# Performance work log

Hardware: AMD Instinct MI355X
Metric: run time of the kernel (lower is better)

The kernel has to match this reference:

```python
import jax, jax.numpy as jnp
import numpy as np

N_NODES = 100000


def setup_inputs() -> dict:
    key = jax.random.key(0)
    k1, k2, k3 = jax.random.split(key, 3)
    x = jax.random.normal(k1, (N_NODES, 128), dtype=jnp.float32)
    edge_index = jax.random.randint(k2, (2, 1600000), 0, N_NODES, dtype=jnp.int64)
    # GCNConv linear weight (hidden, input) and bias; PReLU slope (init 0.25 as in torch)
    W = jax.random.normal(k3, (128, 128), dtype=jnp.float32) * (1.0 / np.sqrt(128))
    b = jnp.zeros((128,), dtype=jnp.float32)
    prelu_a = jnp.full((1,), 0.25, dtype=jnp.float32)
    return {"x": x, "edge_index": edge_index, "W": W, "b": b, "prelu_a": prelu_a}


def reference(x, edge_index, W, b, prelu_a):
    n = x.shape[0]
    # add self loops (as in forward's add_self_loops)
    loop = jnp.arange(n, dtype=edge_index.dtype)
    src = jnp.concatenate([edge_index[0], loop])  # [E+N]
    dst = jnp.concatenate([edge_index[1], loop])
    # linear transform first (small GEMM), then gather/scatter on hidden dim
    h = x @ W.T  # [N, H]
    # symmetric degree normalization 1/sqrt(deg_src * deg_dst), deg = in-degree incl. self-loop
    ones = jnp.ones_like(dst, dtype=h.dtype)
    deg = jax.ops.segment_sum(ones, dst, num_segments=n)
    dinv = jnp.where(deg > 0, jax.lax.rsqrt(deg), 0.0)  # [N]
    norm = dinv[src] * dinv[dst]  # [E+N]
    msg = h[src] * norm[:, None]  # gather + scale, memory-bound
    out = jax.ops.segment_sum(msg, dst, num_segments=n) + b  # scatter-add
    # PReLU (single shared slope); dropout is identity in eval mode
    out = jnp.where(out >= 0, out, prelu_a[0] * out)
    return out
```

## Files before the change

### kernel.cpp

```cpp
#include <hip/hip_runtime.h>
#include <math.h>

#define HDIM 128
#define BSH 9
#define CH 4096
#define GEMM_BLKS 256
#define GSPLIT 160

typedef __attribute__((ext_vector_type(8))) short short8;
typedef __attribute__((ext_vector_type(4))) float f32x4;

__device__ inline unsigned short bf16_hi(float f) {
    return (unsigned short)(__float_as_uint(f) >> 16);
}
__device__ inline unsigned short bf16_rn(float f) {
    unsigned int u = __float_as_uint(f);
    return (unsigned short)((u + 0x7FFF + ((u >> 16) & 1)) >> 16);
}

__global__ __launch_bounds__(256) void prep_kernel(
    const float* __restrict__ W, uint4* __restrict__ Whg, uint4* __restrict__ Wlg) {
    const int t = threadIdx.x;
    for (int idx = t; idx < 2048; idx += 256) {
        const int j = idx >> 4;
        const int c = idx & 15;
        const float4* wp = (const float4*)(W + (size_t)j * HDIM + c * 8);
        float4 va = wp[0], vb = wp[1];
        float vs[8] = {va.x, va.y, va.z, va.w, vb.x, vb.y, vb.z, vb.w};
        unsigned short h[8], l[8];
        #pragma unroll
        for (int k = 0; k < 8; ++k) {
            h[k] = bf16_hi(vs[k]);
            float hf = __uint_as_float((unsigned int)h[k] << 16);
            l[k] = bf16_hi(vs[k] - hf);
        }
        uint4 hch, lch;
        hch.x = (unsigned int)h[0] | ((unsigned int)h[1] << 16);
        hch.y = (unsigned int)h[2] | ((unsigned int)h[3] << 16);
        hch.z = (unsigned int)h[4] | ((unsigned int)h[5] << 16);
        hch.w = (unsigned int)h[6] | ((unsigned int)h[7] << 16);
        lch.x = (unsigned int)l[0] | ((unsigned int)l[1] << 16);
        lch.y = (unsigned int)l[2] | ((unsigned int)l[3] << 16);
        lch.z = (unsigned int)l[4] | ((unsigned int)l[5] << 16);
        lch.w = (unsigned int)l[6] | ((unsigned int)l[7] << 16);
        Whg[idx] = hch;
        Wlg[idx] = lch;
    }
}

__device__ __forceinline__ void gemm_body(
    const float* __restrict__ x, const uint4* __restrict__ Whg,
    const uint4* __restrict__ Wlg, unsigned short* __restrict__ gb, int n,
    int g0, int g1, int bid, int nblk) {
    const int t = threadIdx.x;
    const int wave = t >> 6;
    const int lane = t & 63;
    const int q = lane >> 4;
    const int m = lane & 15;

    for (int grp = g0 + bid; grp < g1; grp += nblk) {
        const int rowbase = (grp << 7) + (wave << 5);

        f32x4 acc[2][8];
        #pragma unroll
        for (int mt = 0; mt < 2; ++mt)
            #pragma unroll
            for (int ct = 0; ct < 8; ++ct)
                acc[mt][ct] = (f32x4){0.f, 0.f, 0.f, 0.f};

        #pragma unroll
        for (int kk = 0; kk < 4; ++kk) {
            short8 ah[2], al[2];
            #pragma unroll
            for (int mt = 0; mt < 2; ++mt) {
                const int r = rowbase + (mt << 4) + m;
                float vs[8];
                if (r < n) {
                    const float4* xp = (const float4*)(x + (size_t)r * HDIM + (kk << 5) + (q << 3));
                    float4 va = xp[0], vb = xp[1];
                    vs[0] = va.x; vs[1] = va.y; vs[2] = va.z; vs[3] = va.w;
                    vs[4] = vb.x; vs[5] = vb.y; vs[6] = vb.z; vs[7] = vb.w;
                } else {
                    #pragma unroll
                    for (int k = 0; k < 8; ++k) vs[k] = 0.f;
                }
                #pragma unroll
                for (int k = 0; k < 8; ++k) {
                    unsigned short h = bf16_hi(vs[k]);
                    float hf = __uint_as_float((unsigned int)h << 16);
                    unsigned short lo = bf16_hi(vs[k] - hf);
                    ah[mt][k] = (short)h;
                    al[mt][k] = (short)lo;
                }
            }
            #pragma unroll
            for (int ct = 0; ct < 8; ++ct) {
                const int nn = (ct << 4) + m;
                const int fidx = (nn << 4) | ((kk << 2) + q);
                short8 bh = *(const short8*)&Whg[fidx];
                short8 bl = *(const short8*)&Wlg[fidx];
                #pragma unroll
                for (int mt = 0; mt < 2; ++mt) {
                    acc[mt][ct] = __builtin_amdgcn_mfma_f32_16x16x32_bf16(ah[mt], bh, acc[mt][ct], 0, 0, 0);
                    acc[mt][ct] = __builtin_amdgcn_mfma_f32_16x16x32_bf16(al[mt], bh, acc[mt][ct], 0, 0, 0);
                    acc[mt][ct] = __builtin_amdgcn_mfma_f32_16x16x32_bf16(ah[mt], bl, acc[mt][ct], 0, 0, 0);
                }
            }
        }

        #pragma unroll
        for (int mt = 0; mt < 2; ++mt) {
            #pragma unroll
            for (int rr = 0; rr < 4; ++rr) {
                const int grow = rowbase + (mt << 4) + (q << 2) + rr;
                if (grow < n) {
                    unsigned short* gp = gb + (size_t)grow * HDIM + m;
                    #pragma unroll
                    for (int ct = 0; ct < 8; ++ct)
                        gp[ct << 4] = bf16_rn(acc[mt][ct][rr]);
                }
            }
        }
    }
}

__device__ __forceinline__ void binA_body(
    const int* __restrict__ dst, int E, int* __restrict__ bcnt,
    int chunk, int* hist) {
    const int t = threadIdx.x;
    const int c0 = chunk * CH;
    hist[t] = 0;
    __syncthreads();
    #pragma unroll
    for (int k = 0; k < CH / 256; ++k) {
        int e = c0 + t + (k << 8);
        if (e < E) atomicAdd(&hist[dst[e] >> BSH], 1);
    }
    __syncthreads();
    if (hist[t] > 0) atomicAdd(&bcnt[t], hist[t]);
}

__device__ __forceinline__ void binB_body(
    const int* __restrict__ ei, int E,
    int* __restrict__ bcur, unsigned int* __restrict__ eb,
    int chunk, int* hist, int* base, int* cur) {
    const int t = threadIdx.x;
    const int c0 = chunk * CH;
    hist[t] = 0;
    __syncthreads();

    int sv[CH / 256], dv[CH / 256];
    #pragma unroll
    for (int k = 0; k < CH / 256; ++k) {
        int e = c0 + t + (k << 8);
        if (e < E) {
            sv[k] = ei[e];
            dv[k] = ei[E + e];
            atomicAdd(&hist[dv[k] >> BSH], 1);
        } else {
            dv[k] = -1;
        }
    }
    __syncthreads();
    if (hist[t] > 0) base[t] = atomicAdd(&bcur[t], hist[t]);
    cur[t] = 0;
    __syncthreads();
    #pragma unroll
    for (int k = 0; k < CH / 256; ++k) {
        if (dv[k] >= 0) {
            int bkt = dv[k] >> BSH;
            int o = atomicAdd(&cur[bkt], 1);
            eb[(size_t)base[bkt] + o] =
                ((unsigned int)(dv[k] & ((1 << BSH) - 1)) << 23) | (unsigned int)sv[k];
        }
    }
}

__global__ __launch_bounds__(256) void fuse1_kernel(
    const int* __restrict__ dst, int E, int* __restrict__ bcnt,
    const float* __restrict__ x, const uint4* __restrict__ Whg,
    const uint4* __restrict__ Wlg, unsigned short* __restrict__ gb,
    int n, int nchunk) {
    __shared__ int s_a[256];
    const int bid = blockIdx.x;
    if (bid < GEMM_BLKS)
        gemm_body(x, Whg, Wlg, gb, n, 0, GSPLIT, bid, GEMM_BLKS);
    else
        binA_body(dst, E, bcnt, bid - GEMM_BLKS, s_a);
}

__global__ __launch_bounds__(256) void scanB_kernel(
    const int* __restrict__ bcnt, int* __restrict__ bbase, int* __restrict__ bcur,
    int NB, int E) {
    __shared__ int s[256];
    const int t = threadIdx.x;
    int v = (t < NB) ? bcnt[t] : 0;
    s[t] = v;
    __syncthreads();
    for (int off = 1; off < 256; off <<= 1) {
        int u = (t >= off) ? s[t - off] : 0;
        __syncthreads();
        s[t] += u;
        __syncthreads();
    }
    int excl = s[t] - v;
    if (t < NB) { bbase[t] = excl; bcur[t] = excl; }
    if (t == 0) bbase[NB] = E;
}

__global__ __launch_bounds__(256) void fuse2_kernel(
    const int* __restrict__ ei, int E, int* __restrict__ bcur,
    unsigned int* __restrict__ eb,
    const float* __restrict__ x, const uint4* __restrict__ Whg,
    const uint4* __restrict__ Wlg, unsigned short* __restrict__ gb,
    int n, int nchunk, int ngroups) {
    __shared__ int s_a[256], s_b[256], s_c[256];
    const int bid = blockIdx.x;
    if (bid < GEMM_BLKS)
        gemm_body(x, Whg, Wlg, gb, n, GSPLIT, ngroups, bid, GEMM_BLKS);
    else
        binB_body(ei, E, bcur, eb, bid - GEMM_BLKS, s_a, s_b, s_c);
}

__global__ __launch_bounds__(512) void binC_kernel(
    const unsigned int* __restrict__ eb, const int* __restrict__ bbase,
    int* __restrict__ row_ptr, float* __restrict__ dinv,
    int* __restrict__ col, int n) {
    __shared__ int hist[512];
    __shared__ int cur[512];
    __shared__ int wsum[8];
    const int t = threadIdx.x;
    const int b = blockIdx.x;
    const int node0 = b << BSH;
    const int e0 = bbase[b];
    const int e1 = bbase[b + 1];

    hist[t] = 0;
    __syncthreads();
    for (int e = e0 + t; e < e1; e += 512)
        atomicAdd(&hist[eb[e] >> 23], 1);
    __syncthreads();
    const int v = hist[t];
    int x = v;
    #pragma unroll
    for (int off = 1; off < 64; off <<= 1) {
        int u = __shfl_up(x, off);
        if ((t & 63) >= off) x += u;
    }
    if ((t & 63) == 63) wsum[t >> 6] = x;
    __syncthreads();
    if (t < 8) {
        int y = wsum[t];
        #pragma unroll
        for (int off = 1; off < 8; off <<= 1) {
            int u = __shfl_up(y, off);
            if (t >= off) y += u;
        }
        wsum[t] = y;
    }
    __syncthreads();
    int excl = x - v + ((t >> 6) ? wsum[(t >> 6) - 1] : 0);

    int node = node0 + t;
    if (node < n) {
        row_ptr[node] = e0 + excl;
        dinv[node] = rsqrtf((float)v + 1.0f);
        if (node == n - 1) row_ptr[n] = e0 + excl + v;
    }
    cur[t] = e0 + excl;
    __syncthreads();
    for (int e = e0 + t; e < e1; e += 512) {
        unsigned int p = eb[e];
        int pos = atomicAdd(&cur[p >> 23], 1);
        col[pos] = (int)(p & 0x7FFFFF);
    }
}

#define EDGE_ACC(d, u) \
    a[0] = fmaf(d, __uint_as_float((u).x << 16), a[0]); \
    a[1] = fmaf(d, __uint_as_float((u).x & 0xffff0000u), a[1]); \
    a[2] = fmaf(d, __uint_as_float((u).y << 16), a[2]); \
    a[3] = fmaf(d, __uint_as_float((u).y & 0xffff0000u), a[3]); \
    a[4] = fmaf(d, __uint_as_float((u).z << 16), a[4]); \
    a[5] = fmaf(d, __uint_as_float((u).z & 0xffff0000u), a[5]); \
    a[6] = fmaf(d, __uint_as_float((u).w << 16), a[6]); \
    a[7] = fmaf(d, __uint_as_float((u).w & 0xffff0000u), a[7]);

__global__ __launch_bounds__(256) void gather_kernel(
    const int* __restrict__ row_ptr, const int* __restrict__ col,
    const uint4* __restrict__ gbr, const float* __restrict__ dinv,
    const float* __restrict__ bias, const float* __restrict__ prelu_a,
    float* __restrict__ out, int n) {
    const int wv = threadIdx.x >> 6;
    const int lane = threadIdx.x & 63;
    const int q = lane >> 4;
    const int l16 = lane & 15;
    const int i = blockIdx.x * 4 + wv;
    if (i >= n) return;

    const int beg = row_ptr[i];
    const int end = row_ptr[i + 1];
    const float di = dinv[i];

    float a[8];
    #pragma unroll
    for (int k = 0; k < 8; ++k) a[k] = 0.f;

    if (q == 0) {
        uint4 u = gbr[(size_t)i * 16 + l16];
        EDGE_ACC(di, u)
    }

    int e = beg + q;
    for (; e + 12 < end; e += 16) {
        int s0 = col[e];
        int s1 = col[e + 4];
        int s2 = col[e + 8];
        int s3 = col[e + 12];
        float d0 = dinv[s0], d1 = dinv[s1], d2 = dinv[s2], d3 = dinv[s3];
        uint4 u0 = gbr[(size_t)s0 * 16 + l16];
        uint4 u1 = gbr[(size_t)s1 * 16 + l16];
        uint4 u2 = gbr[(size_t)s2 * 16 + l16];
        uint4 u3 = gbr[(size_t)s3 * 16 + l16];
        EDGE_ACC(d0, u0)
        EDGE_ACC(d1, u1)
        EDGE_ACC(d2, u2)
        EDGE_ACC(d3, u3)
    }
    for (; e + 4 < end; e += 8) {
        int s0 = col[e];
        int s1 = col[e + 4];
        float d0 = dinv[s0], d1 = dinv[s1];
        uint4 u0 = gbr[(size_t)s0 * 16 + l16];
        uint4 u1 = gbr[(size_t)s1 * 16 + l16];
        EDGE_ACC(d0, u0)
        EDGE_ACC(d1, u1)
    }
    if (e < end) {
        int s = col[e];
        float d = dinv[s];
        uint4 u = gbr[(size_t)s * 16 + l16];
        EDGE_ACC(d, u)
    }

    #pragma unroll
    for (int k = 0; k < 8; ++k) {
        a[k] += __shfl_xor(a[k], 16);
        a[k] += __shfl_xor(a[k], 32);
    }

    const float aa = prelu_a[0];
    const int c0 = (l16 << 3) + (q << 1);
    float2 bb = *(const float2*)(bias + c0);
    float v0 = di * a[(q << 1) + 0] + bb.x;
    float v1 = di * a[(q << 1) + 1] + bb.y;
    v0 = v0 >= 0.f ? v0 : aa * v0;
    v1 = v1 >= 0.f ? v1 : aa * v1;
    *(float2*)(out + (size_t)i * HDIM + c0) = make_float2(v0, v1);
}

extern "C" void kernel_launch(void* const* d_in, const int* in_sizes, int n_in,
                              void* d_out, int out_size, void* d_ws, size_t ws_size,
                              hipStream_t stream) {
    const float* x  = (const float*)d_in[0];
    const int*   ei = (const int*)d_in[1];
    const float* W  = (const float*)d_in[2];
    const float* b  = (const float*)d_in[3];
    const float* pa = (const float*)d_in[4];

    const int n = in_sizes[0] / HDIM;
    const int E = in_sizes[1] / 2;
    const int NB = (n + (1 << BSH) - 1) >> BSH;
    const int ngroups = (n + 127) >> 7;

    float* out = (float*)d_out;

    unsigned short* gb      = (unsigned short*)d_ws;
    unsigned int*   eb      = (unsigned int*)(gb + (size_t)n * HDIM);
    uint4*          Whg     = (uint4*)(eb + (size_t)E);
    uint4*          Wlg     = Whg + 2048;
    float*          dinv    = (float*)(Wlg + 2048);
    int*            row_ptr = (int*)(dinv + n);
    int*            col     = row_ptr + (n + 1);
    int*            bcnt    = col + E;
    int*            bbase   = bcnt + 256;
    int*            bcur    = bbase + 257;

    hipMemsetAsync(bcnt, 0, 256 * sizeof(int), stream);

    const int nchunk = (E + CH - 1) / CH;
    prep_kernel<<<1, 256, 0, stream>>>(W, Whg, Wlg);
    fuse1_kernel<<<GEMM_BLKS + nchunk, 256, 0, stream>>>(ei + E, E, bcnt, x, Whg, Wlg, gb, n, nchunk);
    scanB_kernel<<<1, 256, 0, stream>>>(bcnt, bbase, bcur, NB, E);
    fuse2_kernel<<<GEMM_BLKS + nchunk, 256, 0, stream>>>(ei, E, bcur, eb, x, Whg, Wlg, gb, n, nchunk, ngroups);
    binC_kernel<<<NB, 512, 0, stream>>>(eb, bbase, row_ptr, dinv, col, n);
    gather_kernel<<<(n + 3) / 4, 256, 0, stream>>>(row_ptr, col, (const uint4*)gb, dinv, b, pa, out, n);
}
```

Before: 252.9 us.

## Remove scan kernel by recomputing bucket prefix in binning blocks; halve bucket size

```diff
diff --git a/kernel.cpp b/kernel.cpp
--- a/kernel.cpp
+++ b/kernel.cpp
@@ -2,7 +2,8 @@
 #include <math.h>
 
 #define HDIM 128
-#define BSH 9
+#define BSH 8
+#define LSH 24
 #define CH 4096
 #define GEMM_BLKS 256
 #define GSPLIT 160
@@ -130,6 +131,7 @@
     const int t = threadIdx.x;
     const int c0 = chunk * CH;
     hist[t] = 0;
+    hist[t + 256] = 0;
     __syncthreads();
     #pragma unroll
     for (int k = 0; k < CH / 256; ++k) {
@@ -138,15 +140,17 @@
     }
     __syncthreads();
     if (hist[t] > 0) atomicAdd(&bcnt[t], hist[t]);
+    if (hist[t + 256] > 0) atomicAdd(&bcnt[t + 256], hist[t + 256]);
 }
 
 __device__ __forceinline__ void binB_body(
-    const int* __restrict__ ei, int E,
-    int* __restrict__ bcur, unsigned int* __restrict__ eb,
-    int chunk, int* hist, int* base, int* cur) {
+    const int* __restrict__ ei, int E, const int* __restrict__ bcnt,
+    int* __restrict__ boff, unsigned int* __restrict__ eb,
+    int chunk, int* hist, int* bb, int* base, int* cur, int NB) {
     const int t = threadIdx.x;
     const int c0 = chunk * CH;
     hist[t] = 0;
+    hist[t + 256] = 0;
     __syncthreads();
 
     int sv[CH / 256], dv[CH / 256];
@@ -162,16 +166,38 @@
         }
     }
     __syncthreads();
-    if (hist[t] > 0) base[t] = atomicAdd(&bcur[t], hist[t]);
+
+    if (t < 64) {
+        int carry = 0;
+        #pragma unroll
+        for (int c = 0; c < 512; c += 64) {
+            int idx = c + t;
+            int v = (idx < NB) ? bcnt[idx] : 0;
+            int xs = v;
+            #pragma unroll
+            for (int off = 1; off < 64; off <<= 1) {
+                int u = __shfl_up(xs, off);
+                if (t >= off) xs += u;
+            }
+            bb[idx] = carry + xs - v;
+            carry += __shfl(xs, 63);
+        }
+    }
+    __syncthreads();
+
+    if (hist[t] > 0)       base[t]       = bb[t]       + atomicAdd(&boff[t],       hist[t]);
+    if (hist[t + 256] > 0) base[t + 256] = bb[t + 256] + atomicAdd(&boff[t + 256], hist[t + 256]);
     cur[t] = 0;
-    __syncthreads();
+    cur[t + 256] = 0;
+    __syncthreads();
+
     #pragma unroll
     for (int k = 0; k < CH / 256; ++k) {
         if (dv[k] >= 0) {
             int bkt = dv[k] >> BSH;
             int o = atomicAdd(&cur[bkt], 1);
             eb[(size_t)base[bkt] + o] =
-                ((unsigned int)(dv[k] & ((1 << BSH) - 1)) << 23) | (unsigned int)sv[k];
+                ((unsigned int)(dv[k] & ((1 << BSH) - 1)) << LSH) | (unsigned int)sv[k];
         }
     }
 }
@@ -179,9 +205,8 @@
 __global__ __launch_bounds__(256) void fuse1_kernel(
     const int* __restrict__ dst, int E, int* __restrict__ bcnt,
     const float* __restrict__ x, const uint4* __restrict__ Whg,
-    const uint4* __restrict__ Wlg, unsigned short* __restrict__ gb,
-    int n, int nchunk) {
-    __shared__ int s_a[256];
+    const uint4* __restrict__ Wlg, unsigned short* __restrict__ gb, int n) {
+    __shared__ int s_a[512];
     const int bid = blockIdx.x;
     if (bid < GEMM_BLKS)
         gemm_body(x, Whg, Wlg, gb, n, 0, GSPLIT, bid, GEMM_BLKS);
@@ -189,56 +214,48 @@
         binA_body(dst, E, bcnt, bid - GEMM_BLKS, s_a);
 }
 
-__global__ __launch_bounds__(256) void scanB_kernel(
-    const int* __restrict__ bcnt, int* __restrict__ bbase, int* __restrict__ bcur,
-    int NB, int E) {
-    __shared__ int s[256];
-    const int t = threadIdx.x;
-    int v = (t < NB) ? bcnt[t] : 0;
-    s[t] = v;
-    __syncthreads();
-    for (int off = 1; off < 256; off <<= 1) {
-        int u = (t >= off) ? s[t - off] : 0;
-        __syncthreads();
-        s[t] += u;
-        __syncthreads();
-    }
-    int excl = s[t] - v;
-    if (t < NB) { bbase[t] = excl; bcur[t] = excl; }
-    if (t == 0) bbase[NB] = E;
-}
-
 __global__ __launch_bounds__(256) void fuse2_kernel(
-    const int* __restrict__ ei, int E, int* __restrict__ bcur,
-    unsigned int* __restrict__ eb,
+    const int* __restrict__ ei, int E, const int* __restrict__ bcnt,
+    int* __restrict__ boff, unsigned int* __restrict__ eb,
     const float* __restrict__ x, const uint4* __restrict__ Whg,
     const uint4* __restrict__ Wlg, unsigned short* __restrict__ gb,
-    int n, int nchunk, int ngroups) {
-    __shared__ int s_a[256], s_b[256], s_c[256];
+    int n, int ngroups, int NB) {
+    __shared__ int s_h[512], s_bb[512], s_ba[512], s_cu[512];
     const int bid = blockIdx.x;
     if (bid < GEMM_BLKS)
         gemm_body(x, Whg, Wlg, gb, n, GSPLIT, ngroups, bid, GEMM_BLKS);
     else
-        binB_body(ei, E, bcur, eb, bid - GEMM_BLKS, s_a, s_b, s_c);
-}
-
-__global__ __launch_bounds__(512) void binC_kernel(
-    const unsigned int* __restrict__ eb, const int* __restrict__ bbase,
+        binB_body(ei, E, bcnt, boff, eb, bid - GEMM_BLKS, s_h, s_bb, s_ba, s_cu, NB);
+}
+
+__global__ __launch_bounds__(256) void binC_kernel(
+    const unsigned int* __restrict__ eb, const int* __restrict__ bcnt,
     int* __restrict__ row_ptr, float* __restrict__ dinv,
-    int* __restrict__ col, int n) {
-    __shared__ int hist[512];
-    __shared__ int cur[512];
-    __shared__ int wsum[8];
+    int* __restrict__ col, int n, int NB) {
+    __shared__ int hist[256];
+    __shared__ int cur[256];
+    __shared__ int red[256];
+    __shared__ int wsum[4];
     const int t = threadIdx.x;
     const int b = blockIdx.x;
     const int node0 = b << BSH;
-    const int e0 = bbase[b];
-    const int e1 = bbase[b + 1];
+
+    int part = 0;
+    for (int k = t; k < b; k += 256) part += bcnt[k];
+    red[t] = part;
+    __syncthreads();
+    #pragma unroll
+    for (int off = 128; off > 0; off >>= 1) {
+        if (t < off) red[t] += red[t + off];
+        __syncthreads();
+    }
+    const int e0 = red[0];
+    const int e1 = e0 + bcnt[b];
 
     hist[t] = 0;
     __syncthreads();
-    for (int e = e0 + t; e < e1; e += 512)
-        atomicAdd(&hist[eb[e] >> 23], 1);
+    for (int e = e0 + t; e < e1; e += 256)
+        atomicAdd(&hist[eb[e] >> LSH], 1);
     __syncthreads();
     const int v = hist[t];
     int x = v;
@@ -249,10 +266,10 @@
     }
     if ((t & 63) == 63) wsum[t >> 6] = x;
     __syncthreads();
-    if (t < 8) {
+    if (t < 4) {
         int y = wsum[t];
         #pragma unroll
-        for (int off = 1; off < 8; off <<= 1) {
+        for (int off = 1; off < 4; off <<= 1) {
             int u = __shfl_up(y, off);
             if (t >= off) y += u;
         }
@@ -269,10 +286,10 @@
     }
     cur[t] = e0 + excl;
     __syncthreads();
-    for (int e = e0 + t; e < e1; e += 512) {
+    for (int e = e0 + t; e < e1; e += 256) {
         unsigned int p = eb[e];
-        int pos = atomicAdd(&cur[p >> 23], 1);
-        col[pos] = (int)(p & 0x7FFFFF);
+        int pos = atomicAdd(&cur[p >> LSH], 1);
+        col[pos] = (int)(p & ((1u << LSH) - 1));
     }
 }
 
@@ -383,16 +400,14 @@
     int*            row_ptr = (int*)(dinv + n);
     int*            col     = row_ptr + (n + 1);
     int*            bcnt    = col + E;
-    int*            bbase   = bcnt + 256;
-    int*            bcur    = bbase + 257;
-
-    hipMemsetAsync(bcnt, 0, 256 * sizeof(int), stream);
+    int*            boff    = bcnt + 512;
+
+    hipMemsetAsync(bcnt, 0, 1024 * sizeof(int), stream);
 
     const int nchunk = (E + CH - 1) / CH;
     prep_kernel<<<1, 256, 0, stream>>>(W, Whg, Wlg);
-    fuse1_kernel<<<GEMM_BLKS + nchunk, 256, 0, stream>>>(ei + E, E, bcnt, x, Whg, Wlg, gb, n, nchunk);
-    scanB_kernel<<<1, 256, 0, stream>>>(bcnt, bbase, bcur, NB, E);
-    fuse2_kernel<<<GEMM_BLKS + nchunk, 256, 0, stream>>>(ei, E, bcur, eb, x, Whg, Wlg, gb, n, nchunk, ngroups);
-    binC_kernel<<<NB, 512, 0, stream>>>(eb, bbase, row_ptr, dinv, col, n);
+    fuse1_kernel<<<GEMM_BLKS + nchunk, 256, 0, stream>>>(ei + E, E, bcnt, x, Whg, Wlg, gb, n);
+    fuse2_kernel<<<GEMM_BLKS + nchunk, 256, 0, stream>>>(ei, E, bcnt, boff, eb, x, Whg, Wlg, gb, n, ngroups, NB);
+    binC_kernel<<<NB, 256, 0, stream>>>(eb, bcnt, row_ptr, dinv, col, n, NB);
     gather_kernel<<<(n + 3) / 4, 256, 0, stream>>>(row_ptr, col, (const uint4*)gb, dinv, b, pa, out, n);
 }
```

After: 258.7 us. 1.02x slower.

## Replace two-pass edge bucketing with fixed-capacity buckets and merge GEMM passes

Applied to the files above, without the earlier changes.

```diff
diff --git a/kernel.cpp b/kernel.cpp
--- a/kernel.cpp
+++ b/kernel.cpp
@@ -3,9 +3,9 @@
 
 #define HDIM 128
 #define BSH 9
+#define CAP 10240
 #define CH 4096
 #define GEMM_BLKS 256
-#define GSPLIT 160
 
 typedef __attribute__((ext_vector_type(8))) short short8;
 typedef __attribute__((ext_vector_type(4))) float f32x4;
@@ -19,8 +19,10 @@
 }
 
 __global__ __launch_bounds__(256) void prep_kernel(
-    const float* __restrict__ W, uint4* __restrict__ Whg, uint4* __restrict__ Wlg) {
-    const int t = threadIdx.x;
+    const float* __restrict__ W, uint4* __restrict__ Whg, uint4* __restrict__ Wlg,
+    int* __restrict__ bcur) {
+    const int t = threadIdx.x;
+    bcur[t] = t * CAP;
     for (int idx = t; idx < 2048; idx += 256) {
         const int j = idx >> 4;
         const int c = idx & 15;
@@ -124,22 +126,6 @@
     }
 }
 
-__device__ __forceinline__ void binA_body(
-    const int* __restrict__ dst, int E, int* __restrict__ bcnt,
-    int chunk, int* hist) {
-    const int t = threadIdx.x;
-    const int c0 = chunk * CH;
-    hist[t] = 0;
-    __syncthreads();
-    #pragma unroll
-    for (int k = 0; k < CH / 256; ++k) {
-        int e = c0 + t + (k << 8);
-        if (e < E) atomicAdd(&hist[dst[e] >> BSH], 1);
-    }
-    __syncthreads();
-    if (hist[t] > 0) atomicAdd(&bcnt[t], hist[t]);
-}
-
 __device__ __forceinline__ void binB_body(
     const int* __restrict__ ei, int E,
     int* __restrict__ bcur, unsigned int* __restrict__ eb,
@@ -176,39 +162,7 @@
     }
 }
 
-__global__ __launch_bounds__(256) void fuse1_kernel(
-    const int* __restrict__ dst, int E, int* __restrict__ bcnt,
-    const float* __restrict__ x, const uint4* __restrict__ Whg,
-    const uint4* __restrict__ Wlg, unsigned short* __restrict__ gb,
-    int n, int nchunk) {
-    __shared__ int s_a[256];
-    const int bid = blockIdx.x;
-    if (bid < GEMM_BLKS)
-        gemm_body(x, Whg, Wlg, gb, n, 0, GSPLIT, bid, GEMM_BLKS);
-    else
-        binA_body(dst, E, bcnt, bid - GEMM_BLKS, s_a);
-}
-
-__global__ __launch_bounds__(256) void scanB_kernel(
-    const int* __restrict__ bcnt, int* __restrict__ bbase, int* __restrict__ bcur,
-    int NB, int E) {
-    __shared__ int s[256];
-    const int t = threadIdx.x;
-    int v = (t < NB) ? bcnt[t] : 0;
-    s[t] = v;
-    __syncthreads();
-    for (int off = 1; off < 256; off <<= 1) {
-        int u = (t >= off) ? s[t - off] : 0;
-        __syncthreads();
-        s[t] += u;
-        __syncthreads();
-    }
-    int excl = s[t] - v;
-    if (t < NB) { bbase[t] = excl; bcur[t] = excl; }
-    if (t == 0) bbase[NB] = E;
-}
-
-__global__ __launch_bounds__(256) void fuse2_kernel(
+__global__ __launch_bounds__(256) void fuseAB_kernel(
     const int* __restrict__ ei, int E, int* __restrict__ bcur,
     unsigned int* __restrict__ eb,
     const float* __restrict__ x, const uint4* __restrict__ Whg,
@@ -216,10 +170,28 @@
     int n, int nchunk, int ngroups) {
     __shared__ int s_a[256], s_b[256], s_c[256];
     const int bid = blockIdx.x;
-    if (bid < GEMM_BLKS)
-        gemm_body(x, Whg, Wlg, gb, n, GSPLIT, ngroups, bid, GEMM_BLKS);
+    if (bid < nchunk)
+        binB_body(ei, E, bcur, eb, bid, s_a, s_b, s_c);
     else
-        binB_body(ei, E, bcur, eb, bid - GEMM_BLKS, s_a, s_b, s_c);
+        gemm_body(x, Whg, Wlg, gb, n, 0, ngroups, bid - nchunk, GEMM_BLKS);
+}
+
+__global__ __launch_bounds__(256) void scanB_kernel(
+    const int* __restrict__ bcur, int* __restrict__ bbase, int NB, int E) {
+    __shared__ int s[256];
+    const int t = threadIdx.x;
+    int v = (t < NB) ? (bcur[t] - t * CAP) : 0;
+    s[t] = v;
+    __syncthreads();
+    for (int off = 1; off < 256; off <<= 1) {
+        int u = (t >= off) ? s[t - off] : 0;
+        __syncthreads();
+        s[t] += u;
+        __syncthreads();
+    }
+    int excl = s[t] - v;
+    if (t < NB) bbase[t] = excl;
+    if (t == 0) bbase[NB] = E;
 }
 
 __global__ __launch_bounds__(512) void binC_kernel(
@@ -232,13 +204,14 @@
     const int t = threadIdx.x;
     const int b = blockIdx.x;
     const int node0 = b << BSH;
-    const int e0 = bbase[b];
-    const int e1 = bbase[b + 1];
+    const int o0 = bbase[b];
+    const int cnt = bbase[b + 1] - o0;
+    const size_t s0 = (size_t)b * CAP;
 
     hist[t] = 0;
     __syncthreads();
-    for (int e = e0 + t; e < e1; e += 512)
-        atomicAdd(&hist[eb[e] >> 23], 1);
+    for (int e = t; e < cnt; e += 512)
+        atomicAdd(&hist[eb[s0 + e] >> 23], 1);
     __syncthreads();
     const int v = hist[t];
     int x = v;
@@ -263,14 +236,14 @@
 
     int node = node0 + t;
     if (node < n) {
-        row_ptr[node] = e0 + excl;
+        row_ptr[node] = o0 + excl;
         dinv[node] = rsqrtf((float)v + 1.0f);
-        if (node == n - 1) row_ptr[n] = e0 + excl + v;
-    }
-    cur[t] = e0 + excl;
-    __syncthreads();
-    for (int e = e0 + t; e < e1; e += 512) {
-        unsigned int p = eb[e];
+        if (node == n - 1) row_ptr[n] = o0 + excl + v;
+    }
+    cur[t] = o0 + excl;
+    __syncthreads();
+    for (int e = t; e < cnt; e += 512) {
+        unsigned int p = eb[s0 + e];
         int pos = atomicAdd(&cur[p >> 23], 1);
         col[pos] = (int)(p & 0x7FFFFF);
     }
@@ -377,22 +350,18 @@
 
     unsigned short* gb      = (unsigned short*)d_ws;
     unsigned int*   eb      = (unsigned int*)(gb + (size_t)n * HDIM);
-    uint4*          Whg     = (uint4*)(eb + (size_t)E);
+    uint4*          Whg     = (uint4*)(eb + (size_t)NB * CAP);
     uint4*          Wlg     = Whg + 2048;
     float*          dinv    = (float*)(Wlg + 2048);
     int*            row_ptr = (int*)(dinv + n);
     int*            col     = row_ptr + (n + 1);
-    int*            bcnt    = col + E;
-    int*            bbase   = bcnt + 256;
-    int*            bcur    = bbase + 257;
-
-    hipMemsetAsync(bcnt, 0, 256 * sizeof(int), stream);
+    int*            bcur    = col + E;
+    int*            bbase   = bcur + 256;
 
     const int nchunk = (E + CH - 1) / CH;
-    prep_kernel<<<1, 256, 0, stream>>>(W, Whg, Wlg);
-    fuse1_kernel<<<GEMM_BLKS + nchunk, 256, 0, stream>>>(ei + E, E, bcnt, x, Whg, Wlg, gb, n, nchunk);
-    scanB_kernel<<<1, 256, 0, stream>>>(bcnt, bbase, bcur, NB, E);
-    fuse2_kernel<<<GEMM_BLKS + nchunk, 256, 0, stream>>>(ei, E, bcur, eb, x, Whg, Wlg, gb, n, nchunk, ngroups);
+    prep_kernel<<<1, 256, 0, stream>>>(W, Whg, Wlg, bcur);
+    fuseAB_kernel<<<nchunk + GEMM_BLKS, 256, 0, stream>>>(ei, E, bcur, eb, x, Whg, Wlg, gb, n, nchunk, ngroups);
+    scanB_kernel<<<1, 256, 0, stream>>>(bcur, bbase, NB, E);
     binC_kernel<<<NB, 512, 0, stream>>>(eb, bbase, row_ptr, dinv, col, n);
     gather_kernel<<<(n + 3) / 4, 256, 0, stream>>>(row_ptr, col, (const uint4*)gb, dinv, b, pa, out, n);
 }
```

After: 237.8 us. 6.0% less time.
